# Kernel optimization log

Measured on AMD Instinct MI355X. Metric: run time of the kernel, lower is better.

## Reference

```python
import jax, jax.numpy as jnp
import numpy as np

HIDDEN = 1024
NUM_HEADS = 16
HEAD_DIM = HIDDEN // NUM_HEADS
B, S = 2, 2048


def setup_inputs() -> dict:
    key = jax.random.key(0)
    ks = jax.random.split(key, 7)
    scale = 1.0 / np.sqrt(HIDDEN)
    return {
        "hidden_states": jax.random.normal(ks[0], (B, S, HIDDEN), dtype=jnp.float32),
        "attention_mask": jnp.ones((B, S), dtype=jnp.float32),
        "Wq": jax.random.normal(ks[1], (HIDDEN, HIDDEN), dtype=jnp.float32) * scale,
        "bq": jax.random.normal(ks[2], (HIDDEN,), dtype=jnp.float32) * 0.02,
        "Wk": jax.random.normal(ks[3], (HIDDEN, HIDDEN), dtype=jnp.float32) * scale,
        "bk": jax.random.normal(ks[4], (HIDDEN,), dtype=jnp.float32) * 0.02,
        "Wv": jax.random.normal(ks[5], (HIDDEN, HIDDEN), dtype=jnp.float32) * scale,
        "bv": jax.random.normal(ks[6], (HIDDEN,), dtype=jnp.float32) * 0.02,
    }


def reference(hidden_states, attention_mask, Wq, bq, Wk, bk, Wv, bv):
    # Linear projections (W stored [in, out], equivalent to torch Linear).
    q = hidden_states @ Wq + bq  # [B,S,H]
    k = hidden_states @ Wk + bk
    v = hidden_states @ Wv + bv

    def split_heads(x):  # [B,S,H] -> [B,nh,S,hd]
        return x.reshape(B, S, NUM_HEADS, HEAD_DIM).transpose(0, 2, 1, 3)

    q, k, v = split_heads(q), split_heads(k), split_heads(v)

    scores = jnp.einsum("bhqd,bhkd->bhqk", q, k) / jnp.sqrt(
        jnp.asarray(HEAD_DIM, dtype=q.dtype))
    min_val = jnp.finfo(scores.dtype).min
    ext_mask = (1.0 - attention_mask[:, None, None, :]) * min_val  # [B,1,1,S]
    scores = scores + ext_mask
    probs = jax.nn.softmax(scores, axis=-1)  # eval mode: no dropout
    ctx = jnp.einsum("bhqk,bhkd->bhqd", probs, v)
    ctx = ctx.transpose(0, 2, 1, 3).reshape(B, S, HIDDEN)
    return ctx
```

## Files before the change

kernel.cpp:

```cpp
#include <hip/hip_runtime.h>
#include <hip/hip_bf16.h>
#include <cstddef>
#include <cstdint>

#define HID 1024
#define NHEADS 16
#define HDIM 64
#define BATCH 2
#define SEQ 2048
#define MROWS (BATCH * SEQ)
#define BHT (BATCH * NHEADS)

typedef __attribute__((ext_vector_type(8))) short s8v;
typedef __attribute__((ext_vector_type(4))) float f4v;

__device__ __forceinline__ unsigned short f2bf(float x) {
    union { float f; unsigned int u; } c; c.f = x;
    return (unsigned short)((c.u + 0x7fffu + ((c.u >> 16) & 1u)) >> 16);
}
__device__ __forceinline__ unsigned int pkbf(float a, float b) {
    __hip_bfloat162 h = __float22bfloat162_rn(float2{a, b});
    union { __hip_bfloat162 v; unsigned int u; } c; c.v = h; return c.u;
}
__device__ __forceinline__ float bflo(unsigned int w) {
    union { unsigned int u; float f; } c; c.u = w << 16; return c.f;
}
__device__ __forceinline__ float bfhi(unsigned int w) {
    union { unsigned int u; float f; } c; c.u = w & 0xffff0000u; return c.f;
}

__device__ __forceinline__ void lds_load16(void* lds, const void* g) {
    __builtin_amdgcn_global_load_lds(
        (const __attribute__((address_space(1))) void*)g,
        (__attribute__((address_space(3))) void*)lds, 16, 0, 0);
}

__global__ __launch_bounds__(256) void conv_fused_kernel(
    const float* __restrict__ hs,
    const float* __restrict__ Wq, const float* __restrict__ Wk,
    const float* __restrict__ Wv,
    unsigned short* __restrict__ Ah, unsigned short* __restrict__ WTh)
{
    if (blockIdx.x < 2048) {
        const int idx = (blockIdx.x * 256 + threadIdx.x) * 8;
        float4 v0 = *(const float4*)&hs[idx];
        float4 v1 = *(const float4*)&hs[idx + 4];
        union { unsigned int w[4]; } pk;
        pk.w[0] = pkbf(v0.x, v0.y);
        pk.w[1] = pkbf(v0.z, v0.w);
        pk.w[2] = pkbf(v1.x, v1.y);
        pk.w[3] = pkbf(v1.z, v1.w);
        *(uint4*)&Ah[idx] = *(uint4*)&pk;
    } else {
        const int bid = blockIdx.x - 2048;
        const int z = bid >> 8;
        const int rem = bid & 255;
        const float* W = (z == 0) ? Wq : (z == 1) ? Wk : Wv;
        unsigned short* th = WTh + (size_t)z * HID * HID;

        __shared__ float tile[64][65];
        const int t = threadIdx.x;
        const int kb = (rem >> 4) * 64, nb = (rem & 15) * 64;
        const int c4 = (t & 15) * 4;
        const int r0 = t >> 4;

#pragma unroll
        for (int i = 0; i < 4; ++i) {
            int r = r0 + i * 16;
            float4 v = *(const float4*)&W[(size_t)(kb + r) * HID + nb + c4];
            tile[r][c4 + 0] = v.x; tile[r][c4 + 1] = v.y;
            tile[r][c4 + 2] = v.z; tile[r][c4 + 3] = v.w;
        }
        __syncthreads();
#pragma unroll
        for (int i = 0; i < 4; ++i) {
            int n = r0 + i * 16;
            union { unsigned int w[2]; unsigned long long q; } pk;
            pk.w[0] = pkbf(tile[c4 + 0][n], tile[c4 + 1][n]);
            pk.w[1] = pkbf(tile[c4 + 2][n], tile[c4 + 3][n]);
            *(unsigned long long*)&th[(size_t)(nb + n) * HID + kb + c4] = pk.q;
        }
    }
}

#define GBM 128
#define GBN 128
#define QSCALE 0.18033688011112042f

__global__ __launch_bounds__(256) void qkv_mfma_kernel(
    const unsigned short* __restrict__ Ah, const unsigned short* __restrict__ WTh,
    const float* __restrict__ bq, const float* __restrict__ bk,
    const float* __restrict__ bv,
    unsigned short* __restrict__ Qg, unsigned short* __restrict__ Khi,
    unsigned short* __restrict__ VTg)
{
    const int z = blockIdx.z;
    const float* bias = (z == 0) ? bq : (z == 1) ? bk : bv;
    const unsigned short* Bh = WTh + (size_t)z * HID * HID;

    __shared__ unsigned short AS[2][GBM * 32];
    __shared__ unsigned short BS[2][GBN * 32];

    const int t = threadIdx.x;
    const int wave = t >> 6, lane = t & 63, quad = lane >> 4, l15 = lane & 15;
    const int wm = wave >> 1, wn = wave & 1;
    const int rowBase = blockIdx.x * GBM;
    const int colBase = blockIdx.y * GBN;

    const int srow = lane >> 2;
    const int sc8  = (lane & 3) * 8;
    size_t goffA[2], goffB[2];
#pragma unroll
    for (int it = 0; it < 2; ++it) {
        const int rA = wave * 32 + it * 16;
        goffA[it] = (size_t)(rowBase + rA + srow) * HID + sc8;
        goffB[it] = (size_t)(colBase + rA + srow) * HID + sc8;
    }

    f4v acc[4][4];
#pragma unroll
    for (int mf = 0; mf < 4; ++mf)
#pragma unroll
        for (int nf = 0; nf < 4; ++nf) acc[mf][nf] = (f4v){0.f, 0.f, 0.f, 0.f};

#pragma unroll
    for (int it = 0; it < 2; ++it) {
        const int rA = wave * 32 + it * 16;
        lds_load16(&AS[0][rA * 32], &Ah[goffA[it]]);
        lds_load16(&BS[0][rA * 32], &Bh[goffB[it]]);
    }
    __syncthreads();

    for (int kt = 0; kt < HID / 32; ++kt) {
        const int cur = kt & 1;
        if (kt + 1 < HID / 32) {
            const int nxt = cur ^ 1;
            const int k0 = (kt + 1) * 32;
#pragma unroll
            for (int it = 0; it < 2; ++it) {
                const int rA = wave * 32 + it * 16;
                lds_load16(&AS[nxt][rA * 32], &Ah[goffA[it] + k0]);
                lds_load16(&BS[nxt][rA * 32], &Bh[goffB[it] + k0]);
            }
        }
        s8v af[4], bf[4];
#pragma unroll
        for (int mf = 0; mf < 4; ++mf)
            af[mf] = *(const s8v*)&AS[cur][(wm * 64 + mf * 16 + l15) * 32 + quad * 8];
#pragma unroll
        for (int nf = 0; nf < 4; ++nf)
            bf[nf] = *(const s8v*)&BS[cur][(wn * 64 + nf * 16 + l15) * 32 + quad * 8];
        if (z == 2) {
#pragma unroll
            for (int mf = 0; mf < 4; ++mf)
#pragma unroll
                for (int nf = 0; nf < 4; ++nf)
                    acc[mf][nf] = __builtin_amdgcn_mfma_f32_16x16x32_bf16(af[mf], bf[nf], acc[mf][nf], 0, 0, 0);
        } else {
#pragma unroll
            for (int mf = 0; mf < 4; ++mf)
#pragma unroll
                for (int nf = 0; nf < 4; ++nf)
                    acc[mf][nf] = __builtin_amdgcn_mfma_f32_16x16x32_bf16(bf[nf], af[mf], acc[mf][nf], 0, 0, 0);
        }
        __syncthreads();
    }

    if (z == 2) {
#pragma unroll
        for (int nf = 0; nf < 4; ++nf) {
            const int n = colBase + wn * 64 + nf * 16 + l15;
            const float bb = bias[n];
            const int h = n >> 6, d = n & 63;
#pragma unroll
            for (int mf = 0; mf < 4; ++mf) {
                const int rw0 = rowBase + wm * 64 + mf * 16 + quad * 4;
                const int b = rw0 >> 11;
                const int s0 = rw0 & (SEQ - 1);
                union { unsigned int w[2]; unsigned long long q; } pk;
                pk.w[0] = pkbf(acc[mf][nf][0] + bb, acc[mf][nf][1] + bb);
                pk.w[1] = pkbf(acc[mf][nf][2] + bb, acc[mf][nf][3] + bb);
                *(unsigned long long*)&VTg[((size_t)(b * NHEADS + h) * HDIM + d) * SEQ + s0] = pk.q;
            }
        }
    } else {
        unsigned short* outp = (z == 0) ? Qg : Khi;
        const float scale = (z == 0) ? QSCALE : 1.0f;
#pragma unroll
        for (int nf = 0; nf < 4; ++nf) {
            const int n0 = colBase + wn * 64 + nf * 16 + quad * 4;
            const float4 bb = *(const float4*)&bias[n0];
            const int h = n0 >> 6, d0 = n0 & 63;
#pragma unroll
            for (int mf = 0; mf < 4; ++mf) {
                const int rw = rowBase + wm * 64 + mf * 16 + l15;
                const int b = rw >> 11;
                const int ss = rw & (SEQ - 1);
                union { unsigned int w[2]; unsigned long long q; } pk;
                pk.w[0] = pkbf((acc[mf][nf][0] + bb.x) * scale, (acc[mf][nf][1] + bb.y) * scale);
                pk.w[1] = pkbf((acc[mf][nf][2] + bb.z) * scale, (acc[mf][nf][3] + bb.w) * scale);
                *(unsigned long long*)&outp[((size_t)(b * NHEADS + h) * SEQ + ss) * HDIM + d0] = pk.q;
            }
        }
    }
}

#define BC 64

__global__ __launch_bounds__(256, 2) void attn_mfma_kernel(
    const unsigned short* __restrict__ Qg, const unsigned short* __restrict__ Khi,
    const unsigned short* __restrict__ VTg,
    const float* __restrict__ mask, float* __restrict__ out)
{
    __shared__ unsigned short Kb[2][BC * HDIM];
    __shared__ unsigned short Vb[2][BC * HDIM];
    __shared__ unsigned short Pbuf[4][32 * BC];

    const int t = threadIdx.x;
    const int wave = t >> 6, lane = t & 63, quad = lane >> 4, l15 = lane & 15;
    const int sw = l15 & 7;
    const int bh = blockIdx.x, b = bh >> 4, h = bh & (NHEADS - 1);
    const int qbase = blockIdx.y * 128 + wave * 32;

    const size_t hb = (size_t)bh * SEQ * HDIM;
    const unsigned short* kbase = Khi + hb;
    const unsigned short* vbase = VTg + hb;
    const float* mrow = mask + b * SEQ;

    s8v qh[2][2];
#pragma unroll
    for (int qf = 0; qf < 2; ++qf)
#pragma unroll
        for (int ds = 0; ds < 2; ++ds) {
            size_t off = hb + (size_t)(qbase + qf * 16 + l15) * HDIM + ds * 32 + quad * 8;
            qh[qf][ds] = *(const s8v*)&Qg[off];
        }

    f4v oacc[2][4];
#pragma unroll
    for (int qf = 0; qf < 2; ++qf)
#pragma unroll
        for (int nf = 0; nf < 4; ++nf) oacc[qf][nf] = (f4v){0.f, 0.f, 0.f, 0.f};
    float l_r[2] = {0.f, 0.f};

    const int srow8 = lane >> 3;
    const int sc    = lane & 7;
    int koff[2], voff[2];
#pragma unroll
    for (int it = 0; it < 2; ++it) {
        const int row = (wave * 2 + it) * 8 + srow8;
        const int gx = (sc ^ (row & 7)) * 8;
        koff[it] = row * HDIM + gx;
        voff[it] = row * SEQ + gx;
    }

#pragma unroll
    for (int it = 0; it < 2; ++it) {
        const int i = wave * 2 + it;
        lds_load16(&Kb[0][i * 512], kbase + koff[it]);
        lds_load16(&Vb[0][i * 512], vbase + voff[it]);
    }
    __syncthreads();

    for (int kt = 0; kt < SEQ / BC; ++kt) {
        const int cur = kt & 1;
        if (kt + 1 < SEQ / BC) {
            const int nxt = cur ^ 1;
#pragma unroll
            for (int it = 0; it < 2; ++it) {
                const int i = wave * 2 + it;
                lds_load16(&Kb[nxt][i * 512], kbase + (kt + 1) * BC * HDIM + koff[it]);
                lds_load16(&Vb[nxt][i * 512], vbase + (kt + 1) * BC + voff[it]);
            }
        }
        float4 msv[4];
#pragma unroll
        for (int mf = 0; mf < 4; ++mf)
            msv[mf] = *(const float4*)&mrow[kt * BC + mf * 16 + quad * 4];

        f4v sacc[2][4];
#pragma unroll
        for (int qf = 0; qf < 2; ++qf)
#pragma unroll
            for (int mf = 0; mf < 4; ++mf) sacc[qf][mf] = (f4v){0.f, 0.f, 0.f, 0.f};
#pragma unroll
        for (int mf = 0; mf < 4; ++mf) {
#pragma unroll
            for (int ds = 0; ds < 2; ++ds) {
                s8v kh = *(const s8v*)&Kb[cur][(mf * 16 + l15) * HDIM + (((ds * 4 + quad) ^ sw) * 8)];
#pragma unroll
                for (int qf = 0; qf < 2; ++qf)
                    sacc[qf][mf] = __builtin_amdgcn_mfma_f32_16x16x32_bf16(kh, qh[qf][ds], sacc[qf][mf], 0, 0, 0);
            }
        }

#pragma unroll
        for (int qf = 0; qf < 2; ++qf) {
            float psum = 0.f;
            const int prow = (qf * 16 + l15) * BC;
#pragma unroll
            for (int mf = 0; mf < 4; ++mf) {
                const float* mp = (const float*)&msv[mf];
                float p0 = __builtin_amdgcn_exp2f(sacc[qf][mf][0]) * mp[0];
                float p1 = __builtin_amdgcn_exp2f(sacc[qf][mf][1]) * mp[1];
                float p2 = __builtin_amdgcn_exp2f(sacc[qf][mf][2]) * mp[2];
                float p3 = __builtin_amdgcn_exp2f(sacc[qf][mf][3]) * mp[3];
                union { unsigned int w[2]; unsigned long long q; } pk;
                pk.w[0] = pkbf(p0, p1);
                pk.w[1] = pkbf(p2, p3);
                psum += bflo(pk.w[0]) + bfhi(pk.w[0]) + bflo(pk.w[1]) + bfhi(pk.w[1]);
                const int c16 = (mf * 2 + (quad >> 1)) ^ sw;
                *(unsigned long long*)&Pbuf[wave][prow + c16 * 8 + (quad & 1) * 4] = pk.q;
            }
            l_r[qf] += psum;
        }

#pragma unroll
        for (int ks = 0; ks < 2; ++ks) {
            const int csw = ((ks * 4 + quad) ^ sw) * 8;
            s8v pa0 = *(const s8v*)&Pbuf[wave][(0 * 16 + l15) * BC + csw];
            s8v pa1 = *(const s8v*)&Pbuf[wave][(1 * 16 + l15) * BC + csw];
#pragma unroll
            for (int nf = 0; nf < 4; ++nf) {
                s8v vb = *(const s8v*)&Vb[cur][(nf * 16 + l15) * BC + csw];
                oacc[0][nf] = __builtin_amdgcn_mfma_f32_16x16x32_bf16(pa0, vb, oacc[0][nf], 0, 0, 0);
                oacc[1][nf] = __builtin_amdgcn_mfma_f32_16x16x32_bf16(pa1, vb, oacc[1][nf], 0, 0, 0);
            }
        }
        __syncthreads();
    }

#pragma unroll
    for (int qf = 0; qf < 2; ++qf) {
        float v = l_r[qf];
        v += __shfl_xor(v, 16);
        v += __shfl_xor(v, 32);
        float lv[4];
#pragma unroll
        for (int r = 0; r < 4; ++r)
            lv[r] = 1.0f / __shfl(v, quad * 4 + r);
#pragma unroll
        for (int nf = 0; nf < 4; ++nf)
#pragma unroll
            for (int r = 0; r < 4; ++r) {
                int q = qbase + qf * 16 + quad * 4 + r;
                int d = nf * 16 + l15;
                out[((size_t)b * SEQ + q) * HID + h * HDIM + d] = oacc[qf][nf][r] * lv[r];
            }
    }
}

extern "C" void kernel_launch(void* const* d_in, const int* in_sizes, int n_in,
                              void* d_out, int out_size, void* d_ws, size_t ws_size,
                              hipStream_t stream) {
    const float* hs   = (const float*)d_in[0];
    const float* mask = (const float*)d_in[1];
    const float* Wq   = (const float*)d_in[2];
    const float* bq   = (const float*)d_in[3];
    const float* Wk   = (const float*)d_in[4];
    const float* bk   = (const float*)d_in[5];
    const float* Wv   = (const float*)d_in[6];
    const float* bv   = (const float*)d_in[7];
    float* out = (float*)d_out;

    const size_t N = (size_t)MROWS * HID;
    unsigned short* Qg  = (unsigned short*)d_ws;
    unsigned short* Khi = Qg + N;
    unsigned short* VTg = Qg + 2 * N;
    unsigned short* Ah  = Qg + 3 * N;
    unsigned short* WTh = Qg + 4 * N;

    conv_fused_kernel<<<2048 + 768, 256, 0, stream>>>(hs, Wq, Wk, Wv, Ah, WTh);

    dim3 g1(MROWS / GBM, HID / GBN, 3);
    qkv_mfma_kernel<<<g1, 256, 0, stream>>>(Ah, WTh, bq, bk, bv, Qg, Khi, VTg);

    dim3 g2(BHT, SEQ / 128);
    attn_mfma_kernel<<<g2, 256, 0, stream>>>(Qg, Khi, VTg, mask, out);
}
```

Measured before the change: 199.3 us.

## Fuse Q and K projections per block with swizzled 64-wide K tiles

Reworks the QKV projection GEMM so a single block computes both the Q and K output tiles, reusing each loaded A tile for two weight matrices, while V runs in separate blocks. The K step grows from 32 to 64, the LDS layout gets an XOR swizzle to avoid bank conflicts, and launch bounds now request 2 blocks per CU. Double buffering is removed in favour of a single buffer with syncs on both sides of each load. The Q/K blocks carry twice the accumulators, which raises register pressure and leaves the grid with unbalanced work per block.

After: 174.6 us. 1.14x faster.

```diff
diff --git a/kernel.cpp b/kernel.cpp
--- a/kernel.cpp
+++ b/kernel.cpp
@@ -83,94 +83,147 @@
     }
 }
 
-#define GBM 128
-#define GBN 128
 #define QSCALE 0.18033688011112042f
 
-__global__ __launch_bounds__(256) void qkv_mfma_kernel(
+__global__ __launch_bounds__(256, 2) void qkv_mfma_kernel(
     const unsigned short* __restrict__ Ah, const unsigned short* __restrict__ WTh,
     const float* __restrict__ bq, const float* __restrict__ bk,
     const float* __restrict__ bv,
     unsigned short* __restrict__ Qg, unsigned short* __restrict__ Khi,
     unsigned short* __restrict__ VTg)
 {
-    const int z = blockIdx.z;
-    const float* bias = (z == 0) ? bq : (z == 1) ? bk : bv;
-    const unsigned short* Bh = WTh + (size_t)z * HID * HID;
-
-    __shared__ unsigned short AS[2][GBM * 32];
-    __shared__ unsigned short BS[2][GBN * 32];
-
+    __shared__ unsigned short S[24576];
+    unsigned short* AS = S;
+    unsigned short* B0 = S + 8192;
+    unsigned short* B1 = S + 16384;
+
+    const int z2 = blockIdx.z;
     const int t = threadIdx.x;
     const int wave = t >> 6, lane = t & 63, quad = lane >> 4, l15 = lane & 15;
+    const int sw = l15 & 7;
     const int wm = wave >> 1, wn = wave & 1;
-    const int rowBase = blockIdx.x * GBM;
-    const int colBase = blockIdx.y * GBN;
-
-    const int srow = lane >> 2;
-    const int sc8  = (lane & 3) * 8;
-    size_t goffA[2], goffB[2];
-#pragma unroll
-    for (int it = 0; it < 2; ++it) {
-        const int rA = wave * 32 + it * 16;
-        goffA[it] = (size_t)(rowBase + rA + srow) * HID + sc8;
-        goffB[it] = (size_t)(colBase + rA + srow) * HID + sc8;
-    }
-
-    f4v acc[4][4];
-#pragma unroll
-    for (int mf = 0; mf < 4; ++mf)
-#pragma unroll
-        for (int nf = 0; nf < 4; ++nf) acc[mf][nf] = (f4v){0.f, 0.f, 0.f, 0.f};
-
-#pragma unroll
-    for (int it = 0; it < 2; ++it) {
-        const int rA = wave * 32 + it * 16;
-        lds_load16(&AS[0][rA * 32], &Ah[goffA[it]]);
-        lds_load16(&BS[0][rA * 32], &Bh[goffB[it]]);
-    }
-    __syncthreads();
-
-    for (int kt = 0; kt < HID / 32; ++kt) {
-        const int cur = kt & 1;
-        if (kt + 1 < HID / 32) {
-            const int nxt = cur ^ 1;
-            const int k0 = (kt + 1) * 32;
-#pragma unroll
-            for (int it = 0; it < 2; ++it) {
-                const int rA = wave * 32 + it * 16;
-                lds_load16(&AS[nxt][rA * 32], &Ah[goffA[it] + k0]);
-                lds_load16(&BS[nxt][rA * 32], &Bh[goffB[it] + k0]);
-            }
-        }
-        s8v af[4], bf[4];
+    const int rowBase = blockIdx.x * 128;
+    const int colBase = blockIdx.y * 128;
+
+    const int srow8 = lane >> 3;
+    const int sc    = lane & 7;
+
+    const unsigned short* BhQ = WTh;
+    const unsigned short* BhK = WTh + (size_t)HID * HID;
+    const unsigned short* BhV = WTh + (size_t)2 * HID * HID;
+
+    size_t goffA[4], goffB[4];
+#pragma unroll
+    for (int it = 0; it < 4; ++it) {
+        const int row = (wave * 4 + it) * 8 + srow8;
+        const int gx = (sc ^ (row & 7)) * 8;
+        goffA[it] = (size_t)(rowBase + row) * HID + gx;
+        goffB[it] = (size_t)(colBase + row) * HID + gx;
+    }
+
+    if (z2 == 0) {
+        f4v accq[4][4], acck[4][4];
 #pragma unroll
         for (int mf = 0; mf < 4; ++mf)
-            af[mf] = *(const s8v*)&AS[cur][(wm * 64 + mf * 16 + l15) * 32 + quad * 8];
-#pragma unroll
-        for (int nf = 0; nf < 4; ++nf)
-            bf[nf] = *(const s8v*)&BS[cur][(wn * 64 + nf * 16 + l15) * 32 + quad * 8];
-        if (z == 2) {
-#pragma unroll
-            for (int mf = 0; mf < 4; ++mf)
+#pragma unroll
+            for (int nf = 0; nf < 4; ++nf) {
+                accq[mf][nf] = (f4v){0.f, 0.f, 0.f, 0.f};
+                acck[mf][nf] = (f4v){0.f, 0.f, 0.f, 0.f};
+            }
+
+        for (int kt = 0; kt < HID / 64; ++kt) {
+            const int k0 = kt * 64;
+            __syncthreads();
+#pragma unroll
+            for (int it = 0; it < 4; ++it) {
+                lds_load16(&AS[(wave * 4 + it) * 512], &Ah[goffA[it] + k0]);
+                lds_load16(&B0[(wave * 4 + it) * 512], &BhQ[goffB[it] + k0]);
+                lds_load16(&B1[(wave * 4 + it) * 512], &BhK[goffB[it] + k0]);
+            }
+            __syncthreads();
+
+#pragma unroll
+            for (int kk = 0; kk < 2; ++kk) {
+                const int csw = ((kk * 4 + quad) ^ sw) * 8;
+                s8v af[4], bfq[4], bfk[4];
+#pragma unroll
+                for (int mf = 0; mf < 4; ++mf)
+                    af[mf] = *(const s8v*)&AS[(wm * 64 + mf * 16 + l15) * 64 + csw];
+#pragma unroll
+                for (int nf = 0; nf < 4; ++nf) {
+                    bfq[nf] = *(const s8v*)&B0[(wn * 64 + nf * 16 + l15) * 64 + csw];
+                    bfk[nf] = *(const s8v*)&B1[(wn * 64 + nf * 16 + l15) * 64 + csw];
+                }
+#pragma unroll
+                for (int mf = 0; mf < 4; ++mf)
+#pragma unroll
+                    for (int nf = 0; nf < 4; ++nf) {
+                        accq[mf][nf] = __builtin_amdgcn_mfma_f32_16x16x32_bf16(bfq[nf], af[mf], accq[mf][nf], 0, 0, 0);
+                        acck[mf][nf] = __builtin_amdgcn_mfma_f32_16x16x32_bf16(bfk[nf], af[mf], acck[mf][nf], 0, 0, 0);
+                    }
+            }
+        }
+
+#pragma unroll
+        for (int nf = 0; nf < 4; ++nf) {
+            const int n0 = colBase + wn * 64 + nf * 16 + quad * 4;
+            const float4 bbq = *(const float4*)&bq[n0];
+            const float4 bbk = *(const float4*)&bk[n0];
+            const int h = n0 >> 6, d0 = n0 & 63;
+#pragma unroll
+            for (int mf = 0; mf < 4; ++mf) {
+                const int rw = rowBase + wm * 64 + mf * 16 + l15;
+                const int b = rw >> 11;
+                const int ss = rw & (SEQ - 1);
+                const size_t base = ((size_t)(b * NHEADS + h) * SEQ + ss) * HDIM + d0;
+                union { unsigned int w[2]; unsigned long long q; } pk;
+                pk.w[0] = pkbf((accq[mf][nf][0] + bbq.x) * QSCALE, (accq[mf][nf][1] + bbq.y) * QSCALE);
+                pk.w[1] = pkbf((accq[mf][nf][2] + bbq.z) * QSCALE, (accq[mf][nf][3] + bbq.w) * QSCALE);
+                *(unsigned long long*)&Qg[base] = pk.q;
+                pk.w[0] = pkbf(acck[mf][nf][0] + bbk.x, acck[mf][nf][1] + bbk.y);
+                pk.w[1] = pkbf(acck[mf][nf][2] + bbk.z, acck[mf][nf][3] + bbk.w);
+                *(unsigned long long*)&Khi[base] = pk.q;
+            }
+        }
+    } else {
+        f4v acc[4][4];
+#pragma unroll
+        for (int mf = 0; mf < 4; ++mf)
+#pragma unroll
+            for (int nf = 0; nf < 4; ++nf) acc[mf][nf] = (f4v){0.f, 0.f, 0.f, 0.f};
+
+        for (int kt = 0; kt < HID / 64; ++kt) {
+            const int k0 = kt * 64;
+            __syncthreads();
+#pragma unroll
+            for (int it = 0; it < 4; ++it) {
+                lds_load16(&AS[(wave * 4 + it) * 512], &Ah[goffA[it] + k0]);
+                lds_load16(&B0[(wave * 4 + it) * 512], &BhV[goffB[it] + k0]);
+            }
+            __syncthreads();
+
+#pragma unroll
+            for (int kk = 0; kk < 2; ++kk) {
+                const int csw = ((kk * 4 + quad) ^ sw) * 8;
+                s8v af[4], bf[4];
+#pragma unroll
+                for (int mf = 0; mf < 4; ++mf)
+                    af[mf] = *(const s8v*)&AS[(wm * 64 + mf * 16 + l15) * 64 + csw];
 #pragma unroll
                 for (int nf = 0; nf < 4; ++nf)
-                    acc[mf][nf] = __builtin_amdgcn_mfma_f32_16x16x32_bf16(af[mf], bf[nf], acc[mf][nf], 0, 0, 0);
-        } else {
-#pragma unroll
-            for (int mf = 0; mf < 4; ++mf)
-#pragma unroll
-                for (int nf = 0; nf < 4; ++nf)
-                    acc[mf][nf] = __builtin_amdgcn_mfma_f32_16x16x32_bf16(bf[nf], af[mf], acc[mf][nf], 0, 0, 0);
-        }
-        __syncthreads();
-    }
-
-    if (z == 2) {
+                    bf[nf] = *(const s8v*)&B0[(wn * 64 + nf * 16 + l15) * 64 + csw];
+#pragma unroll
+                for (int mf = 0; mf < 4; ++mf)
+#pragma unroll
+                    for (int nf = 0; nf < 4; ++nf)
+                        acc[mf][nf] = __builtin_amdgcn_mfma_f32_16x16x32_bf16(af[mf], bf[nf], acc[mf][nf], 0, 0, 0);
+            }
+        }
+
 #pragma unroll
         for (int nf = 0; nf < 4; ++nf) {
             const int n = colBase + wn * 64 + nf * 16 + l15;
-            const float bb = bias[n];
+            const float bb = bv[n];
             const int h = n >> 6, d = n & 63;
 #pragma unroll
             for (int mf = 0; mf < 4; ++mf) {
@@ -181,25 +234,6 @@
                 pk.w[0] = pkbf(acc[mf][nf][0] + bb, acc[mf][nf][1] + bb);
                 pk.w[1] = pkbf(acc[mf][nf][2] + bb, acc[mf][nf][3] + bb);
                 *(unsigned long long*)&VTg[((size_t)(b * NHEADS + h) * HDIM + d) * SEQ + s0] = pk.q;
-            }
-        }
-    } else {
-        unsigned short* outp = (z == 0) ? Qg : Khi;
-        const float scale = (z == 0) ? QSCALE : 1.0f;
-#pragma unroll
-        for (int nf = 0; nf < 4; ++nf) {
-            const int n0 = colBase + wn * 64 + nf * 16 + quad * 4;
-            const float4 bb = *(const float4*)&bias[n0];
-            const int h = n0 >> 6, d0 = n0 & 63;
-#pragma unroll
-            for (int mf = 0; mf < 4; ++mf) {
-                const int rw = rowBase + wm * 64 + mf * 16 + l15;
-                const int b = rw >> 11;
-                const int ss = rw & (SEQ - 1);
-                union { unsigned int w[2]; unsigned long long q; } pk;
-                pk.w[0] = pkbf((acc[mf][nf][0] + bb.x) * scale, (acc[mf][nf][1] + bb.y) * scale);
-                pk.w[1] = pkbf((acc[mf][nf][2] + bb.z) * scale, (acc[mf][nf][3] + bb.w) * scale);
-                *(unsigned long long*)&outp[((size_t)(b * NHEADS + h) * SEQ + ss) * HDIM + d0] = pk.q;
             }
         }
     }
@@ -372,7 +406,7 @@
 
     conv_fused_kernel<<<2048 + 768, 256, 0, stream>>>(hs, Wq, Wk, Wv, Ah, WTh);
 
-    dim3 g1(MROWS / GBM, HID / GBN, 3);
+    dim3 g1(MROWS / 128, HID / 128, 2);
     qkv_mfma_kernel<<<g1, 256, 0, stream>>>(Ah, WTh, bq, bk, bv, Qg, Khi, VTg);
 
     dim3 g2(BHT, SEQ / 128);
```
